# Performance work log

Measured on AMD Instinct MI355X. Metric: run time of the kernel, lower is better.

The kernel has to match this reference:

```python
import jax, jax.numpy as jnp
import numpy as np

N_NODES = 100000
DIM_IN = 128
N_PAIRS = 500000
D2 = 2 * DIM_IN  # concat dim = 256


def setup_inputs() -> dict:
    key = jax.random.key(0)
    k_x, k_idx, k_w1, k_b1, k_w2, k_b2 = jax.random.split(key, 6)
    x = jax.random.normal(k_x, (N_NODES, DIM_IN), dtype=jnp.float32)
    junc_index_pair = jax.random.randint(k_idx, (N_PAIRS, 2), 0, N_NODES, dtype=jnp.int64)
    # MLP: Linear(2d -> 2d) + ReLU, then Linear(2d -> 1), both with bias
    s1 = 1.0 / np.sqrt(D2)
    W1 = jax.random.uniform(k_w1, (D2, D2), minval=-s1, maxval=s1, dtype=jnp.float32)
    b1 = jax.random.uniform(k_b1, (D2,), minval=-s1, maxval=s1, dtype=jnp.float32)
    W2 = jax.random.uniform(k_w2, (D2, 1), minval=-s1, maxval=s1, dtype=jnp.float32)
    b2 = jax.random.uniform(k_b2, (1,), minval=-s1, maxval=s1, dtype=jnp.float32)
    return {"x": x, "junc_index_pair": junc_index_pair,
            "W1": W1, "b1": b1, "W2": W2, "b2": b2}


def reference(x, junc_index_pair, W1, b1, W2, b2):
    # gather both endpoints: [n_pairs, dim_in] each
    node_start = x[junc_index_pair[:, 0]]
    node_end = x[junc_index_pair[:, 1]]
    h = jnp.concatenate((node_start, node_end), axis=1)  # [n_pairs, 2*dim_in]
    h = jax.nn.relu(h @ W1 + b1)                          # [n_pairs, 2*dim_in]
    pred = h @ W2 + b2                                    # [n_pairs, 1]
    return pred.squeeze()                                 # [n_pairs]
```

## Files before the change

### kernel.cpp

```cpp
#include <hip/hip_runtime.h>
#include <hip/hip_bf16.h>
#include <stdint.h>

#define NPAIRS 500000
#define NNODES 100000
#define DIM    128
#define D2     256

typedef __bf16 bf16;
typedef __bf16 bf16x8 __attribute__((ext_vector_type(8)));
typedef __bf16 bf16x4 __attribute__((ext_vector_type(4)));
typedef float  f32x4  __attribute__((ext_vector_type(4)));

__global__ void pack_w1p(const float* __restrict__ W1, bf16* __restrict__ w1p) {
    int t = blockIdx.x * 256 + threadIdx.x;
    int lane = t & 63;
    int kks = (t >> 6) & 3;
    int cg  = t >> 8;
    int l15 = lane & 15, lg = lane >> 4;
    int np = cg * 16 + l15;
    int k0 = kks * 32 + lg * 8;
    const float* src = (np < D2) ? (W1 + (long)k0 * D2 + np)
                                 : (W1 + (long)(k0 + 128) * D2 + (np - D2));
    bf16x8 v;
#pragma unroll
    for (int j = 0; j < 8; ++j) v[j] = (bf16)src[(long)j * D2];
    *(bf16x8*)((char*)w1p + ((long)t << 4)) = v;
}

__launch_bounds__(512, 8)
__global__ void gemm_uvq(const float* __restrict__ x,
                         const bf16*  __restrict__ w1p,
                         int8_t*      __restrict__ UV8,
                         float*       __restrict__ Sq) {
    __shared__ char xt[64 * 256];
    __shared__ char hs[64 * 256];
    int tid  = threadIdx.x;
    int wave = tid >> 6, lane = tid & 63;
    int l15 = lane & 15, lg = lane >> 4;
    long nb = (long)blockIdx.x * 64;

#pragma unroll
    for (int it = 0; it < 2; ++it) {
        int task = it * 512 + tid;
        int r = task >> 4, c = task & 15;
        long node = nb + r;
        const float* src = x + (node < NNODES ? node : 0) * DIM + c * 8;
        float4 a = ((const float4*)src)[0];
        float4 b = ((const float4*)src)[1];
        bf16x8 v;
        v[0]=(bf16)a.x; v[1]=(bf16)a.y; v[2]=(bf16)a.z; v[3]=(bf16)a.w;
        v[4]=(bf16)b.x; v[5]=(bf16)b.y; v[6]=(bf16)b.z; v[7]=(bf16)b.w;
        *(bf16x8*)(xt + r * 256 + ((c * 16) ^ ((r & 15) << 4))) = v;
    }
    __syncthreads();

#pragma unroll 1
    for (int p = 0; p < 4; ++p) {
        f32x4 acc[4];
#pragma unroll
        for (int nf = 0; nf < 4; ++nf) acc[nf] = (f32x4){0.f, 0.f, 0.f, 0.f};

        int cg = p * 8 + wave;
#pragma unroll
        for (int kks = 0; kks < 4; ++kks) {
            bf16x8 wf = *(const bf16x8*)((const char*)w1p +
                            (((cg * 4 + kks) * 64 + lane) << 4));
            int kbyte = kks * 64 + lg * 16;
#pragma unroll
            for (int nf = 0; nf < 4; ++nf) {
                int r = nf * 16 + l15;
                bf16x8 xf = *(const bf16x8*)(xt + r * 256 + (kbyte ^ ((r & 15) << 4)));
                acc[nf] = __builtin_amdgcn_mfma_f32_16x16x32_bf16(wf, xf, acc[nf], 0, 0, 0);
            }
        }

#pragma unroll
        for (int nf = 0; nf < 4; ++nf) {
            int row  = nf * 16 + l15;
            int col8 = wave * 32 + lg * 8;
            bf16x4 o;
            o[0] = (bf16)acc[nf][0];
            o[1] = (bf16)acc[nf][1];
            o[2] = (bf16)acc[nf][2];
            o[3] = (bf16)acc[nf][3];
            *(bf16x4*)(hs + row * 256 + (col8 ^ ((row & 15) << 4))) = o;
        }
        __syncthreads();

#pragma unroll
        for (int it = 0; it < 4; ++it) {
            int row = it * 16 + wave * 2 + (lane >> 5);
            int c   = (lane & 31) * 8;
            bf16x4 hv = *(const bf16x4*)(hs + row * 256 + (c ^ ((row & 15) << 4)));
            float f0 = (float)hv[0], f1 = (float)hv[1], f2 = (float)hv[2], f3 = (float)hv[3];
            float m = fmaxf(fmaxf(fabsf(f0), fabsf(f1)), fmaxf(fabsf(f2), fabsf(f3)));
            m = fmaxf(m, __shfl_xor(m, 1));
            m = fmaxf(m, __shfl_xor(m, 2));
            m = fmaxf(m, __shfl_xor(m, 4));
            m = fmaxf(m, __shfl_xor(m, 8));
            m = fmaxf(m, __shfl_xor(m, 16));
            float scale = m * (1.0f / 127.0f);
            float rs = (m > 1e-20f) ? 127.0f / m : 0.f;
            int q0 = (int)__builtin_rintf(f0 * rs);
            int q1 = (int)__builtin_rintf(f1 * rs);
            int q2 = (int)__builtin_rintf(f2 * rs);
            int q3 = (int)__builtin_rintf(f3 * rs);
            uint32_t packed = (uint32_t)(q0 & 255) | ((uint32_t)(q1 & 255) << 8)
                            | ((uint32_t)(q2 & 255) << 16) | ((uint32_t)(q3 & 255) << 24);
            long node = nb + row;
            if (node < NNODES) {
                *(uint32_t*)((char*)UV8 + node * 512 + p * 128 + (lane & 31) * 4) = packed;
                if ((lane & 31) == 0) Sq[node * 4 + p] = scale;
            }
        }
        __syncthreads();
    }
}

__launch_bounds__(512)
__global__ void pair_pred8(const int8_t* __restrict__ UV8,
                           const float* __restrict__ Sq,
                           const int* __restrict__ junc,
                           const float* __restrict__ b1, const float* __restrict__ w2,
                           const float* __restrict__ b2, float* __restrict__ out) {
    int tid = threadIdx.x;
    int lane = tid & 63, half = lane >> 5, l31 = lane & 31;
    int stripe = l31 >> 4;
    long gw = (long)blockIdx.x * 8 + (tid >> 6);
    float b1c[8], w2c[8];
#pragma unroll
    for (int e = 0; e < 8; ++e) {
        int col = l31 * 8 + e;
        b1c[e] = b1[col];
        w2c[e] = w2[col];
    }
    float b2v = b2[0];
    const long HALF = NPAIRS / 2;
    for (long q = gw; q < HALF; q += 8192) {
        long p = 2 * q + half;
        int2 ij = ((const int2*)junc)[p];
        uint2 ur = *(const uint2*)(UV8 + (long)ij.x * 512 + l31 * 8);
        uint2 vr = *(const uint2*)(UV8 + (long)ij.y * 512 + 256 + l31 * 8);
        float su = Sq[ij.x * 4 + stripe];
        float sv = Sq[ij.y * 4 + 2 + stripe];
        float s = 0.f;
#pragma unroll
        for (int e = 0; e < 8; ++e) {
            int du = (e < 4) ? (int)ur.x : (int)ur.y;
            int dv = (e < 4) ? (int)vr.x : (int)vr.y;
            int sh = 24 - 8 * (e & 3);
            int ub = (du << sh) >> 24;
            int vb = (dv << sh) >> 24;
            float h = fmaf(su, (float)ub, fmaf(sv, (float)vb, b1c[e]));
            s = fmaf(fmaxf(h, 0.f), w2c[e], s);
        }
        s += __shfl_xor(s, 1);
        s += __shfl_xor(s, 2);
        s += __shfl_xor(s, 4);
        s += __shfl_xor(s, 8);
        s += __shfl_xor(s, 16);
        if (l31 == 0) out[p] = s + b2v;
    }
}

__global__ void pack_w1(const float* __restrict__ W1, bf16* __restrict__ w1f) {
    int t = blockIdx.x * 256 + threadIdx.x;
    int lane = t & 63;
    int kk = (t >> 6) & 7;
    int cg = t >> 9;
    int l15 = lane & 15, lg = lane >> 4;
    bf16x8 v;
#pragma unroll
    for (int j = 0; j < 8; ++j)
        v[j] = (bf16)W1[(long)(kk * 32 + lg * 8 + j) * D2 + cg * 16 + l15];
    *(bf16x8*)((char*)w1f + ((long)t << 4)) = v;
}

__launch_bounds__(512, 2)
__global__ void fused_fb(const float* __restrict__ x, const int* __restrict__ junc,
                         const bf16* __restrict__ w1f, const float* __restrict__ b1,
                         const float* __restrict__ w2p, const float* __restrict__ b2,
                         float* __restrict__ out) {
    __shared__ char  atile[128 * 512];
    __shared__ float outp[4][128];
    int tid  = threadIdx.x;
    int wave = tid >> 6, lane = tid & 63;
    int l15 = lane & 15, lg = lane >> 4;
    int wr = wave >> 2, wc = wave & 3;
    long base_p = (long)blockIdx.x * 128;

    float bb[4][4], ww[4][4];
#pragma unroll
    for (int m = 0; m < 4; ++m)
#pragma unroll
        for (int r = 0; r < 4; ++r) {
            int hc = wc * 64 + m * 16 + lg * 4 + r;
            bb[m][r] = b1[hc];
            ww[m][r] = w2p[hc];
        }
#pragma unroll
    for (int it = 0; it < 8; ++it) {
        int task  = it * 512 + tid;
        int nr = task >> 4, chunk = task & 15;
        int r = nr >> 1, side = nr & 1;
        long p = base_p + r;
        int idx = (p < NPAIRS) ? junc[p * 2 + side] : 0;
        const float4* src = (const float4*)(x + (long)idx * DIM + chunk * 8);
        float4 a = src[0], b = src[1];
        bf16x8 v;
        v[0]=(bf16)a.x; v[1]=(bf16)a.y; v[2]=(bf16)a.z; v[3]=(bf16)a.w;
        v[4]=(bf16)b.x; v[5]=(bf16)b.y; v[6]=(bf16)b.z; v[7]=(bf16)b.w;
        int bir = side * 256 + chunk * 16;
        *(bf16x8*)(atile + r * 512 + (bir ^ ((r & 31) << 4))) = v;
    }
    __syncthreads();

    f32x4 acc[4][4];
#pragma unroll
    for (int m = 0; m < 4; ++m)
#pragma unroll
        for (int n = 0; n < 4; ++n)
            acc[m][n] = (f32x4){0.f, 0.f, 0.f, 0.f};
#pragma unroll
    for (int kk = 0; kk < 8; ++kk) {
        bf16x8 xf[4];
        int kbyte = kk * 64 + lg * 16;
#pragma unroll
        for (int n = 0; n < 4; ++n) {
            int r = wr * 64 + n * 16 + l15;
            xf[n] = *(const bf16x8*)(atile + r * 512 + (kbyte ^ ((r & 31) << 4)));
        }
#pragma unroll
        for (int m = 0; m < 4; ++m) {
            bf16x8 wf = *(const bf16x8*)((const char*)w1f +
                            ((((wc * 4 + m) * 8 + kk) * 64 + lane) << 4));
#pragma unroll
            for (int n = 0; n < 4; ++n)
                acc[m][n] = __builtin_amdgcn_mfma_f32_16x16x32_bf16(wf, xf[n], acc[m][n], 0, 0, 0);
        }
    }
#pragma unroll
    for (int n = 0; n < 4; ++n) {
        float s = 0.f;
#pragma unroll
        for (int m = 0; m < 4; ++m)
#pragma unroll
            for (int r = 0; r < 4; ++r)
                s = fmaf(fmaxf(acc[m][n][r] + bb[m][r], 0.f), ww[m][r], s);
        s += __shfl_xor(s, 16);
        s += __shfl_xor(s, 32);
        if (lg == 0) outp[wc][wr * 64 + n * 16 + l15] = s;
    }
    __syncthreads();
    if (tid < 128) {
        long p = base_p + tid;
        if (p < NPAIRS)
            out[p] = b2[0] + outp[0][tid] + outp[1][tid] + outp[2][tid] + outp[3][tid];
    }
}

extern "C" void kernel_launch(void* const* d_in, const int* in_sizes, int n_in,
                              void* d_out, int out_size, void* d_ws, size_t ws_size,
                              hipStream_t stream) {
    const float* x    = (const float*)d_in[0];
    const int*   junc = (const int*)  d_in[1];
    const float* W1   = (const float*)d_in[2];
    const float* b1   = (const float*)d_in[3];
    const float* W2   = (const float*)d_in[4];
    const float* b2   = (const float*)d_in[5];
    float* out = (float*)d_out;

    const size_t UV8_B = (size_t)NNODES * 512;
    const size_t SQ_B  = (size_t)NNODES * 16;
    const size_t NEED  = UV8_B + SQ_B + 131072;

    if (ws_size >= NEED) {
        char* base = (char*)d_ws;
        int8_t* UV8 = (int8_t*)base;
        float*  Sq  = (float*)(base + UV8_B);
        bf16*   w1p = (bf16*) (base + UV8_B + SQ_B);
        hipLaunchKernelGGL(pack_w1p, dim3(32), dim3(256), 0, stream, W1, w1p);
        hipLaunchKernelGGL(gemm_uvq, dim3((NNODES + 63) / 64), dim3(512), 0, stream,
                           x, w1p, UV8, Sq);
        hipLaunchKernelGGL(pair_pred8, dim3(1024), dim3(512), 0, stream,
                           UV8, Sq, junc, b1, W2, b2, out);
    } else {
        bf16* w1f = (bf16*)d_ws;
        hipLaunchKernelGGL(pack_w1, dim3(32), dim3(256), 0, stream, W1, w1f);
        hipLaunchKernelGGL(fused_fb, dim3((NPAIRS + 127) / 128), dim3(512), 0, stream,
                           x, junc, w1f, b1, W2, b2, out);
    }
}
```

Measured before the change: 100.4 us.

## Quantize GEMM output in registers and widen pair gather to 16-byte loads

The gemm kernel now computes per-row absmax directly from the MFMA accumulators with shuffles and an LDS atomicMax. It quantizes to int8 in registers and stages the packed bytes in a smaller swizzled LDS tile, so the stores to UV8 become coalesced 16-byte writes. This drops the bf16 round-trip through shared memory and adds clamping to the ±127 range. The pair kernel now uses 16 lanes per pair with uint4 loads in place of 32 lanes with uint2 loads, which halves the lanes per pair and shortens the reduction.

```diff
diff --git a/kernel.cpp b/kernel.cpp
--- a/kernel.cpp
+++ b/kernel.cpp
@@ -9,7 +9,6 @@
 
 typedef __bf16 bf16;
 typedef __bf16 bf16x8 __attribute__((ext_vector_type(8)));
-typedef __bf16 bf16x4 __attribute__((ext_vector_type(4)));
 typedef float  f32x4  __attribute__((ext_vector_type(4)));
 
 __global__ void pack_w1p(const float* __restrict__ W1, bf16* __restrict__ w1p) {
@@ -34,7 +33,8 @@
                          int8_t*      __restrict__ UV8,
                          float*       __restrict__ Sq) {
     __shared__ char xt[64 * 256];
-    __shared__ char hs[64 * 256];
+    __shared__ char hs8[64 * 128];
+    __shared__ int  smx[64];
     int tid  = threadIdx.x;
     int wave = tid >> 6, lane = tid & 63;
     int l15 = lane & 15, lg = lane >> 4;
@@ -57,6 +57,8 @@
 
 #pragma unroll 1
     for (int p = 0; p < 4; ++p) {
+        if (tid < 64) smx[tid] = 0;
+
         f32x4 acc[4];
 #pragma unroll
         for (int nf = 0; nf < 4; ++nf) acc[nf] = (f32x4){0.f, 0.f, 0.f, 0.f};
@@ -74,47 +76,47 @@
                 acc[nf] = __builtin_amdgcn_mfma_f32_16x16x32_bf16(wf, xf, acc[nf], 0, 0, 0);
             }
         }
+        __syncthreads();
 
 #pragma unroll
         for (int nf = 0; nf < 4; ++nf) {
-            int row  = nf * 16 + l15;
-            int col8 = wave * 32 + lg * 8;
-            bf16x4 o;
-            o[0] = (bf16)acc[nf][0];
-            o[1] = (bf16)acc[nf][1];
-            o[2] = (bf16)acc[nf][2];
-            o[3] = (bf16)acc[nf][3];
-            *(bf16x4*)(hs + row * 256 + (col8 ^ ((row & 15) << 4))) = o;
+            float m = fmaxf(fmaxf(fabsf(acc[nf][0]), fabsf(acc[nf][1])),
+                            fmaxf(fabsf(acc[nf][2]), fabsf(acc[nf][3])));
+            m = fmaxf(m, __shfl_xor(m, 16));
+            m = fmaxf(m, __shfl_xor(m, 32));
+            if (lg == 0) atomicMax(&smx[nf * 16 + l15], __float_as_int(m));
         }
         __syncthreads();
 
 #pragma unroll
-        for (int it = 0; it < 4; ++it) {
-            int row = it * 16 + wave * 2 + (lane >> 5);
-            int c   = (lane & 31) * 8;
-            bf16x4 hv = *(const bf16x4*)(hs + row * 256 + (c ^ ((row & 15) << 4)));
-            float f0 = (float)hv[0], f1 = (float)hv[1], f2 = (float)hv[2], f3 = (float)hv[3];
-            float m = fmaxf(fmaxf(fabsf(f0), fabsf(f1)), fmaxf(fabsf(f2), fabsf(f3)));
-            m = fmaxf(m, __shfl_xor(m, 1));
-            m = fmaxf(m, __shfl_xor(m, 2));
-            m = fmaxf(m, __shfl_xor(m, 4));
-            m = fmaxf(m, __shfl_xor(m, 8));
-            m = fmaxf(m, __shfl_xor(m, 16));
-            float scale = m * (1.0f / 127.0f);
-            float rs = (m > 1e-20f) ? 127.0f / m : 0.f;
-            int q0 = (int)__builtin_rintf(f0 * rs);
-            int q1 = (int)__builtin_rintf(f1 * rs);
-            int q2 = (int)__builtin_rintf(f2 * rs);
-            int q3 = (int)__builtin_rintf(f3 * rs);
-            uint32_t packed = (uint32_t)(q0 & 255) | ((uint32_t)(q1 & 255) << 8)
-                            | ((uint32_t)(q2 & 255) << 16) | ((uint32_t)(q3 & 255) << 24);
+        for (int nf = 0; nf < 4; ++nf) {
+            int row = nf * 16 + l15;
+            float m2 = __int_as_float(smx[row]);
+            float rs = (m2 > 1e-20f) ? 127.0f * __builtin_amdgcn_rcpf(m2) : 0.f;
+            uint32_t packed = 0;
+#pragma unroll
+            for (int r = 0; r < 4; ++r) {
+                int q = (int)__builtin_rintf(acc[nf][r] * rs);
+                q = q > 127 ? 127 : (q < -127 ? -127 : q);
+                packed |= ((uint32_t)(q & 255)) << (8 * r);
+            }
+            int col = (wave * 16 + lg * 4) ^ ((row & 7) << 4);
+            *(uint32_t*)(hs8 + row * 128 + col) = packed;
+        }
+        __syncthreads();
+
+        {
+            int row = tid >> 3, c16 = (tid & 7) << 4;
+            uint4 v = *(const uint4*)(hs8 + row * 128 + (c16 ^ ((row & 7) << 4)));
             long node = nb + row;
-            if (node < NNODES) {
-                *(uint32_t*)((char*)UV8 + node * 512 + p * 128 + (lane & 31) * 4) = packed;
-                if ((lane & 31) == 0) Sq[node * 4 + p] = scale;
-            }
-        }
-        __syncthreads();
+            if (node < NNODES)
+                *(uint4*)((char*)UV8 + node * 512 + p * 128 + c16) = v;
+        }
+        if (tid < 64) {
+            long node = nb + tid;
+            if (node < NNODES)
+                Sq[node * 4 + p] = __int_as_float(smx[tid]) * (1.0f / 127.0f);
+        }
     }
 }
 
@@ -125,42 +127,44 @@
                            const float* __restrict__ b1, const float* __restrict__ w2,
                            const float* __restrict__ b2, float* __restrict__ out) {
     int tid = threadIdx.x;
-    int lane = tid & 63, half = lane >> 5, l31 = lane & 31;
-    int stripe = l31 >> 4;
-    long gw = (long)blockIdx.x * 8 + (tid >> 6);
-    float b1c[8], w2c[8];
-#pragma unroll
-    for (int e = 0; e < 8; ++e) {
-        int col = l31 * 8 + e;
+    int l15 = tid & 15;
+    long qid = (((long)blockIdx.x * 512 + tid) >> 4);
+    int st = l15 >> 3;
+    float b1c[16], w2c[16];
+#pragma unroll
+    for (int e = 0; e < 16; ++e) {
+        int col = l15 * 16 + e;
         b1c[e] = b1[col];
         w2c[e] = w2[col];
     }
     float b2v = b2[0];
-    const long HALF = NPAIRS / 2;
-    for (long q = gw; q < HALF; q += 8192) {
-        long p = 2 * q + half;
+    for (long p = qid; p < NPAIRS; p += 32768) {
         int2 ij = ((const int2*)junc)[p];
-        uint2 ur = *(const uint2*)(UV8 + (long)ij.x * 512 + l31 * 8);
-        uint2 vr = *(const uint2*)(UV8 + (long)ij.y * 512 + 256 + l31 * 8);
-        float su = Sq[ij.x * 4 + stripe];
-        float sv = Sq[ij.y * 4 + 2 + stripe];
+        uint4 u4 = *(const uint4*)(UV8 + (long)ij.x * 512 + l15 * 16);
+        uint4 v4 = *(const uint4*)(UV8 + (long)ij.y * 512 + 256 + l15 * 16);
+        float su = Sq[ij.x * 4 + st];
+        float sv = Sq[ij.y * 4 + 2 + st];
         float s = 0.f;
-#pragma unroll
-        for (int e = 0; e < 8; ++e) {
-            int du = (e < 4) ? (int)ur.x : (int)ur.y;
-            int dv = (e < 4) ? (int)vr.x : (int)vr.y;
-            int sh = 24 - 8 * (e & 3);
-            int ub = (du << sh) >> 24;
-            int vb = (dv << sh) >> 24;
-            float h = fmaf(su, (float)ub, fmaf(sv, (float)vb, b1c[e]));
-            s = fmaf(fmaxf(h, 0.f), w2c[e], s);
-        }
+#define DEC(ud, vd, eb)                                                        \
+        {                                                                      \
+            _Pragma("unroll")                                                  \
+            for (int b = 0; b < 4; ++b) {                                      \
+                int ub = (int)((ud) << (24 - 8 * b)) >> 24;                    \
+                int vb = (int)((vd) << (24 - 8 * b)) >> 24;                    \
+                float h = fmaf(su, (float)ub, fmaf(sv, (float)vb, b1c[(eb) + b])); \
+                s = fmaf(fmaxf(h, 0.f), w2c[(eb) + b], s);                     \
+            }                                                                  \
+        }
+        DEC(u4.x, v4.x, 0)
+        DEC(u4.y, v4.y, 4)
+        DEC(u4.z, v4.z, 8)
+        DEC(u4.w, v4.w, 12)
+#undef DEC
         s += __shfl_xor(s, 1);
         s += __shfl_xor(s, 2);
         s += __shfl_xor(s, 4);
         s += __shfl_xor(s, 8);
-        s += __shfl_xor(s, 16);
-        if (l31 == 0) out[p] = s + b2v;
+        if (l15 == 0) out[p] = s + b2v;
     }
 }
 
```

After: 93.58 us, median of 2. 6.8% less time.
